# Kernel tuning notes

Measured on AMD Instinct MI355X. Metric: run time of the kernel, lower is better.

## Reference

```python
import jax, jax.numpy as jnp
import numpy as np

CROSSOVER_MAGNITUDE = 0.3
MUTATION_FACTOR = 0.3

B, A, H = 16, 512, 8  # batch, activation_size (== dim_emb), n_head


def setup_inputs() -> dict:
    key = jax.random.key(0)
    ks = jax.random.split(key, 11)
    d = A
    s = 0.02  # small init scale for weights
    return {
        "Q": jax.random.normal(ks[0], (B, A, A), jnp.float32),
        "K": jax.random.normal(ks[1], (B, A, A), jnp.float32),
        "V": jax.random.normal(ks[2], (B, A), jnp.float32),
        "WQ_w": jax.random.normal(ks[3], (d, d), jnp.float32) * s,
        "WQ_b": jax.random.normal(ks[4], (d,), jnp.float32) * s,
        "WK_w": jax.random.normal(ks[5], (d, d), jnp.float32) * s,
        "WK_b": jax.random.normal(ks[6], (d,), jnp.float32) * s,
        "WV_w": jax.random.normal(ks[7], (d, d), jnp.float32) * s,
        "WV_b": jax.random.normal(ks[8], (d,), jnp.float32) * s,
        "WO_w": jax.random.normal(ks[9], (d, d * H), jnp.float32) * s,
        "WO_b": jax.random.normal(ks[10], (d,), jnp.float32) * s,
    }


def _attention_core(Qp, Kp, Vp, WO_w, WO_b):
    # Qp, Kp: (B, A, A) projected; identical across heads in the original
    # (heads are copies stacked before shared Linear), so compute once
    # and broadcast. Vp: (B, A).
    rkey = jax.random.key(42)
    kp, km, kr1, kr2 = jax.random.split(rkey, 4)

    am0 = jnp.einsum('bji,bjk->bik', Qp, Kp) / jnp.sqrt(jnp.float32(8.0))
    am = jnp.broadcast_to(am0[:, None], (B, H, A, A))  # (B,H,A,A)

    def mutate(a):
        # elementwise multiply by U(1-mf, 1+mf) noise
        m = jax.random.uniform(km, a.shape, jnp.float32,
                               1.0 - MUTATION_FACTOR, 1.0 + MUTATION_FACTOR)
        return a * m

    def crossover(a):
        # swap the tail segments [c:] of two random rows per (batch, head)
        c = A - int(A * CROSSOVER_MAGNITUDE)
        r1 = jax.random.randint(kr1, (B, H), 0, A)
        r2 = jax.random.randint(kr2, (B, H), 0, A)
        bi = jnp.arange(B)[:, None]
        hi = jnp.arange(H)[None, :]
        tails = a[..., c:]                     # (B,H,A,A-c)
        t1 = tails[bi, hi, r1]                 # (B,H,A-c)
        t2 = tails[bi, hi, r2]
        tails = tails.at[bi, hi, r1].set(t2).at[bi, hi, r2].set(t1)
        return jnp.concatenate([a[..., :c], tails], axis=-1)

    p = jax.random.uniform(kp, ())
    am = jax.lax.cond(p <= 0.6, mutate, crossover, am)

    attn = jax.nn.softmax(am, axis=-1)               # (B,H,A,A)
    out = jnp.einsum('bhij,bj->bhi', attn, Vp)       # attn @ V[...,None] squeezed
    out = out.reshape(B, H * A)
    return out @ WO_w.T + WO_b                       # (B, A)


def reference(Q, K, V, WQ_w, WQ_b, WK_w, WK_b, WV_w, WV_b, WO_w, WO_b):
    Qp = Q @ WQ_w.T + WQ_b   # (B,A,A), same for every head
    Kp = K @ WK_w.T + WK_b
    Vp = V @ WV_w.T + WV_b   # (B,A)
    return _attention_core(Qp, Kp, Vp, WO_w, WO_b)
```

## Files before the change

### kernel.cpp

```cpp
#include <hip/hip_runtime.h>
#include <stdint.h>
#include <string.h>

#define B_ 16
#define A_ 512
#define H_ 8
#define C_CROSS 359
#define LDSTRIDE 40

typedef short short8 __attribute__((ext_vector_type(8)));
typedef unsigned short us8 __attribute__((ext_vector_type(8)));
typedef float floatx4 __attribute__((ext_vector_type(4)));

__host__ __device__ __forceinline__ uint32_t rotl32(uint32_t x, int r) {
#ifdef __HIP_DEVICE_COMPILE__
  return __builtin_amdgcn_alignbit(x, x, 32 - r);
#else
  return (x << r) | (x >> (32 - r));
#endif
}

__host__ __device__ __forceinline__ void tf2x32(uint32_t k0, uint32_t k1,
                                                uint32_t x0, uint32_t x1,
                                                uint32_t& o0, uint32_t& o1) {
  uint32_t ks2 = k0 ^ k1 ^ 0x1BD11BDAu;
  x0 += k0; x1 += k1;
#define TFR(r) { x0 += x1; x1 = rotl32(x1, r); x1 ^= x0; }
  TFR(13) TFR(15) TFR(26) TFR(6)   x0 += k1;  x1 += ks2 + 1u;
  TFR(17) TFR(29) TFR(16) TFR(24)  x0 += ks2; x1 += k0 + 2u;
  TFR(13) TFR(15) TFR(26) TFR(6)   x0 += k0;  x1 += k1 + 3u;
  TFR(17) TFR(29) TFR(16) TFR(24)  x0 += k1;  x1 += ks2 + 4u;
  TFR(13) TFR(15) TFR(26) TFR(6)   x0 += ks2; x1 += k0 + 5u;
#undef TFR
  o0 = x0; o1 = x1;
}

__host__ __device__ __forceinline__ float bits2u01(uint32_t bits) {
  uint32_t v = (bits >> 9) | 0x3f800000u;
  float f;
#ifdef __HIP_DEVICE_COMPILE__
  f = __uint_as_float(v);
#else
  memcpy(&f, &v, 4);
#endif
  return f - 1.0f;
}

__device__ __forceinline__ float exp2_native(float x) {
  float r;
  asm("v_exp_f32 %0, %1\n\ts_nop 0" : "=v"(r) : "v"(x));
  return r;
}

__device__ __forceinline__ void tsplit(float x, short& h, short& l) {
  uint32_t u = __float_as_uint(x);
  float hf = __uint_as_float(u & 0xffff0000u);
  h = (short)(u >> 16);
  l = (short)(__float_as_uint(x - hf) >> 16);
}

__device__ __forceinline__ void tsplit8(const float4& v0, const float4& v1,
                                        short8& h, short8& l) {
  float xs[8] = {v0.x, v0.y, v0.z, v0.w, v1.x, v1.y, v1.z, v1.w};
#pragma unroll
  for (int j = 0; j < 8; ++j) {
    short hh, ll;
    tsplit(xs[j], hh, ll);
    h[j] = hh; l[j] = ll;
  }
}

__device__ __forceinline__ void genmul_chunk(ushort* __restrict__ mbits, int chunk,
                                             uint32_t km0, uint32_t km1) {
  int t = threadIdx.x;
  uint32_t base = (uint32_t)chunk * 16384u;
#pragma unroll
  for (int j = 0; j < 8; ++j) {
    uint32_t L0 = base + (uint32_t)j * 2048u + (uint32_t)t * 8u;
    us8 out;
#pragma unroll
    for (int q = 0; q < 8; ++q) {
      uint32_t o0, o1;
      tf2x32(km0, km1, 0u, L0 + (uint32_t)q, o0, o1);
      out[q] = (unsigned short)((o0 ^ o1) >> 16);
    }
    *(us8*)(mbits + L0) = out;
  }
}

__global__ __launch_bounds__(256) void presplitW(
    const float* __restrict__ Wq, ushort* __restrict__ WqH, ushort* __restrict__ WqL,
    const float* __restrict__ Wk, ushort* __restrict__ WkH, ushort* __restrict__ WkL) {
  int gid = blockIdx.x * 256 + threadIdx.x;
  int z = gid >> 15;
  size_t e0 = (size_t)(gid & 32767) * 8;
  const float* W = z ? Wk : Wq;
  ushort* WH = z ? WkH : WqH;
  ushort* WL = z ? WkL : WqL;
  float4 v0 = *(const float4*)(W + e0);
  float4 v1 = *(const float4*)(W + e0 + 4);
  short8 h8, l8;
  tsplit8(v0, v1, h8, l8);
  *(short8*)(WH + e0) = h8;
  *(short8*)(WL + e0) = l8;
}

__global__ __launch_bounds__(256, 2) void lin3(
    const float* __restrict__ Xq,
    const ushort* __restrict__ WqH, const ushort* __restrict__ WqL,
    const float* __restrict__ bq, ushort* __restrict__ QptH, ushort* __restrict__ QptL,
    const float* __restrict__ Xk,
    const ushort* __restrict__ WkH, const ushort* __restrict__ WkL,
    const float* __restrict__ bk, ushort* __restrict__ KptH, ushort* __restrict__ KptL,
    ushort* __restrict__ mbits, int genOff, uint32_t km0, uint32_t km1) {
  int bid = blockIdx.x;
  if (bid >= 512) {
    genmul_chunk(mbits, genOff + (bid - 512), km0, km1);
    return;
  }
  int z = bid >> 8;
  int rem = bid & 255;
  int ti = rem >> 2, tn = rem & 3;
  const float* X = z ? Xk : Xq;
  const ushort* WH = z ? WkH : WqH;
  const ushort* WL = z ? WkL : WqL;
  const float* bias = z ? bk : bq;
  ushort* OH = z ? KptH : QptH;
  ushort* OL = z ? KptL : QptL;

  __shared__ __align__(16) char smem[40960];
  ushort (*Ah)[LDSTRIDE] = (ushort(*)[LDSTRIDE])(smem);
  ushort (*Al)[LDSTRIDE] = (ushort(*)[LDSTRIDE])(smem + 10240);
  ushort (*Bh)[LDSTRIDE] = (ushort(*)[LDSTRIDE])(smem + 20480);
  ushort (*Bl)[LDSTRIDE] = (ushort(*)[LDSTRIDE])(smem + 30720);
  uint32_t (*cs)[132] = (uint32_t(*)[132])(smem);

  int tid = threadIdx.x;
  int w = tid >> 6, lane = tid & 63, quad = lane >> 4, l16 = lane & 15;
  int wm = (w >> 1) * 64, wn = (w & 1) * 64;
  int m0 = ti * 128;
  int n0 = tn * 128;

  float bv[4];
#pragma unroll
  for (int nt = 0; nt < 4; ++nt) bv[nt] = bias[n0 + wn + nt * 16 + l16];

  const float* pX[2];
  const ushort* pWH[2];
  const ushort* pWL[2];
  int mW[2], kgW[2];
#pragma unroll
  for (int g = 0; g < 2; ++g) {
    int gid = g * 256 + tid;
    int m = gid >> 2, kg = gid & 3;
    mW[g] = m; kgW[g] = kg;
    pX[g] = X + (size_t)(m0 + m) * 512 + kg * 8;
    size_t woff = (size_t)(n0 + m) * 512 + kg * 8;
    pWH[g] = WH + woff;
    pWL[g] = WL + woff;
  }

  float4 ra[2][2];
  short8 rbh[2], rbl[2];
#pragma unroll
  for (int g = 0; g < 2; ++g) {
    ra[g][0] = *(const float4*)(pX[g]);
    ra[g][1] = *(const float4*)(pX[g] + 4);
    rbh[g] = *(const short8*)(pWH[g]);
    rbl[g] = *(const short8*)(pWL[g]);
  }

  floatx4 acc[4][4] = {};

  for (int k0 = 0; k0 < 512; k0 += 32) {
    __syncthreads();
#pragma unroll
    for (int g = 0; g < 2; ++g) {
      short8 h8, l8;
      tsplit8(ra[g][0], ra[g][1], h8, l8);
      *(short8*)&Ah[mW[g]][kgW[g] * 8] = h8;
      *(short8*)&Al[mW[g]][kgW[g] * 8] = l8;
      *(short8*)&Bh[mW[g]][kgW[g] * 8] = rbh[g];
      *(short8*)&Bl[mW[g]][kgW[g] * 8] = rbl[g];
    }
    __syncthreads();
    if (k0 < 480) {
      int kn = k0 + 32;
#pragma unroll
      for (int g = 0; g < 2; ++g) {
        ra[g][0] = *(const float4*)(pX[g] + kn);
        ra[g][1] = *(const float4*)(pX[g] + kn + 4);
        rbh[g] = *(const short8*)(pWH[g] + kn);
        rbl[g] = *(const short8*)(pWL[g] + kn);
      }
    }
    short8 fAh[4], fAl[4], fBh[4], fBl[4];
#pragma unroll
    for (int t4 = 0; t4 < 4; ++t4) {
      int ma = wm + t4 * 16 + l16;
      int nb = wn + t4 * 16 + l16;
      fAh[t4] = *(const short8*)&Ah[ma][quad * 8];
      fAl[t4] = *(const short8*)&Al[ma][quad * 8];
      fBh[t4] = *(const short8*)&Bh[nb][quad * 8];
      fBl[t4] = *(const short8*)&Bl[nb][quad * 8];
    }
#pragma unroll
    for (int mt = 0; mt < 4; ++mt)
#pragma unroll
      for (int nt = 0; nt < 4; ++nt) {
        acc[mt][nt] = __builtin_amdgcn_mfma_f32_16x16x32_bf16(fAh[mt], fBh[nt], acc[mt][nt], 0, 0, 0);
        acc[mt][nt] = __builtin_amdgcn_mfma_f32_16x16x32_bf16(fAh[mt], fBl[nt], acc[mt][nt], 0, 0, 0);
        acc[mt][nt] = __builtin_amdgcn_mfma_f32_16x16x32_bf16(fAl[mt], fBh[nt], acc[mt][nt], 0, 0, 0);
      }
  }

  __syncthreads();
  int bb = m0 >> 9, i0 = m0 & 511;
  for (int p = 0; p < 2; ++p) {
    if ((w & 1) == p) {
#pragma unroll
      for (int mt = 0; mt < 4; ++mt)
#pragma unroll
        for (int nt = 0; nt < 4; ++nt)
#pragma unroll
          for (int rr = 0; rr < 4; ++rr) {
            float val = acc[mt][nt][rr] + bv[nt];
            uint32_t u = __float_as_uint(val);
            uint32_t hi = u & 0xffff0000u;
            uint32_t lo = __float_as_uint(val - __uint_as_float(hi)) >> 16;
            cs[nt * 16 + l16][wm + mt * 16 + quad * 4 + rr] = hi | lo;
          }
    }
    __syncthreads();
    {
      int col_l = tid >> 2, iseg = (tid & 3) * 32;
      int d = n0 + p * 64 + col_l;
      size_t obase = ((size_t)(bb * 512 + d)) * 512 + i0 + iseg;
      ushort* oh = OH + obase;
      ushort* ol = OL + obase;
#pragma unroll
      for (int sgi = 0; sgi < 4; ++sgi) {
        short8 hv, lv;
#pragma unroll
        for (int j = 0; j < 8; ++j) {
          uint32_t v = cs[col_l][iseg + sgi * 8 + j];
          hv[j] = (short)(v >> 16);
          lv[j] = (short)(v & 0xffffu);
        }
        *(short8*)(oh + sgi * 8) = hv;
        *(short8*)(ol + sgi * 8) = lv;
      }
    }
    __syncthreads();
  }
}

__global__ __launch_bounds__(256, 2) void lin_mfma2(
    const float* __restrict__ Xq, const float* __restrict__ Wq,
    const float* __restrict__ bq, ushort* __restrict__ QptH, ushort* __restrict__ QptL,
    const float* __restrict__ Xk, const float* __restrict__ Wk,
    const float* __restrict__ bk, ushort* __restrict__ KptH, ushort* __restrict__ KptL) {
  int bid = blockIdx.x;
  int z = bid >> 8;
  int rem = bid & 255;
  int ti = rem >> 2, tn = rem & 3;
  const float* X = z ? Xk : Xq;
  const float* W = z ? Wk : Wq;
  const float* bias = z ? bk : bq;
  ushort* OH = z ? KptH : QptH;
  ushort* OL = z ? KptL : QptL;

  __shared__ __align__(16) char smem[40960];
  ushort (*Ah)[LDSTRIDE] = (ushort(*)[LDSTRIDE])(smem);
  ushort (*Al)[LDSTRIDE] = (ushort(*)[LDSTRIDE])(smem + 10240);
  ushort (*Bh)[LDSTRIDE] = (ushort(*)[LDSTRIDE])(smem + 20480);
  ushort (*Bl)[LDSTRIDE] = (ushort(*)[LDSTRIDE])(smem + 30720);
  uint32_t (*cs)[132] = (uint32_t(*)[132])(smem);

  int tid = threadIdx.x;
  int w = tid >> 6, lane = tid & 63, quad = lane >> 4, l16 = lane & 15;
  int wm = (w >> 1) * 64, wn = (w & 1) * 64;
  int m0 = ti * 128;
  int n0 = tn * 128;

  float bv[4];
#pragma unroll
  for (int nt = 0; nt < 4; ++nt) bv[nt] = bias[n0 + wn + nt * 16 + l16];

  const float* pX[2];
  const float* pW[2];
  int mW[2], kgW[2];
#pragma unroll
  for (int g = 0; g < 2; ++g) {
    int gid = g * 256 + tid;
    int m = gid >> 2, kg = gid & 3;
    mW[g] = m; kgW[g] = kg;
    pX[g] = X + (size_t)(m0 + m) * 512 + kg * 8;
    pW[g] = W + (size_t)(n0 + m) * 512 + kg * 8;
  }

  float4 ra[2][2], rb[2][2];
#pragma unroll
  for (int g = 0; g < 2; ++g) {
    ra[g][0] = *(const float4*)(pX[g]);
    ra[g][1] = *(const float4*)(pX[g] + 4);
    rb[g][0] = *(const float4*)(pW[g]);
    rb[g][1] = *(const float4*)(pW[g] + 4);
  }

  floatx4 acc[4][4] = {};

  for (int k0 = 0; k0 < 512; k0 += 32) {
    __syncthreads();
#pragma unroll
    for (int g = 0; g < 2; ++g) {
      short8 h8, l8;
      tsplit8(ra[g][0], ra[g][1], h8, l8);
      *(short8*)&Ah[mW[g]][kgW[g] * 8] = h8;
      *(short8*)&Al[mW[g]][kgW[g] * 8] = l8;
      tsplit8(rb[g][0], rb[g][1], h8, l8);
      *(short8*)&Bh[mW[g]][kgW[g] * 8] = h8;
      *(short8*)&Bl[mW[g]][kgW[g] * 8] = l8;
    }
    __syncthreads();
    if (k0 < 480) {
      int kn = k0 + 32;
#pragma unroll
      for (int g = 0; g < 2; ++g) {
        ra[g][0] = *(const float4*)(pX[g] + kn);
        ra[g][1] = *(const float4*)(pX[g] + kn + 4);
        rb[g][0] = *(const float4*)(pW[g] + kn);
        rb[g][1] = *(const float4*)(pW[g] + kn + 4);
      }
    }
    short8 fAh[4], fAl[4], fBh[4], fBl[4];
#pragma unroll
    for (int t4 = 0; t4 < 4; ++t4) {
      int ma = wm + t4 * 16 + l16;
      int nb = wn + t4 * 16 + l16;
      fAh[t4] = *(const short8*)&Ah[ma][quad * 8];
      fAl[t4] = *(const short8*)&Al[ma][quad * 8];
      fBh[t4] = *(const short8*)&Bh[nb][quad * 8];
      fBl[t4] = *(const short8*)&Bl[nb][quad * 8];
    }
#pragma unroll
    for (int mt = 0; mt < 4; ++mt)
#pragma unroll
      for (int nt = 0; nt < 4; ++nt) {
        acc[mt][nt] = __builtin_amdgcn_mfma_f32_16x16x32_bf16(fAh[mt], fBh[nt], acc[mt][nt], 0, 0, 0);
        acc[mt][nt] = __builtin_amdgcn_mfma_f32_16x16x32_bf16(fAh[mt], fBl[nt], acc[mt][nt], 0, 0, 0);
        acc[mt][nt] = __builtin_amdgcn_mfma_f32_16x16x32_bf16(fAl[mt], fBh[nt], acc[mt][nt], 0, 0, 0);
      }
  }

  __syncthreads();
  int bb = m0 >> 9, i0 = m0 & 511;
  for (int p = 0; p < 2; ++p) {
    if ((w & 1) == p) {
#pragma unroll
      for (int mt = 0; mt < 4; ++mt)
#pragma unroll
        for (int nt = 0; nt < 4; ++nt)
#pragma unroll
          for (int rr = 0; rr < 4; ++rr) {
            float val = acc[mt][nt][rr] + bv[nt];
            uint32_t u = __float_as_uint(val);
            uint32_t hi = u & 0xffff0000u;
            uint32_t lo = __float_as_uint(val - __uint_as_float(hi)) >> 16;
            cs[nt * 16 + l16][wm + mt * 16 + quad * 4 + rr] = hi | lo;
          }
    }
    __syncthreads();
    {
      int col_l = tid >> 2, iseg = (tid & 3) * 32;
      int d = n0 + p * 64 + col_l;
      size_t obase = ((size_t)(bb * 512 + d)) * 512 + i0 + iseg;
      ushort* oh = OH + obase;
      ushort* ol = OL + obase;
#pragma unroll
      for (int sgi = 0; sgi < 4; ++sgi) {
        short8 hv, lv;
#pragma unroll
        for (int j = 0; j < 8; ++j) {
          uint32_t v = cs[col_l][iseg + sgi * 8 + j];
          hv[j] = (short)(v >> 16);
          lv[j] = (short)(v & 0xffffu);
        }
        *(short8*)(oh + sgi * 8) = hv;
        *(short8*)(ol + sgi * 8) = lv;
      }
    }
    __syncthreads();
  }
}

__global__ __launch_bounds__(256, 2) void am3(
    const ushort* __restrict__ QH, const ushort* __restrict__ QL,
    const ushort* __restrict__ KH, const ushort* __restrict__ KL,
    float* __restrict__ am0,
    ushort* __restrict__ mbits, int genOff, uint32_t km0, uint32_t km1) {
  int bid = blockIdx.x;
  if (bid >= 256) {
    genmul_chunk(mbits, genOff + (bid - 256), km0, km1);
    return;
  }
  int xcd = bid & 7, slot = bid >> 3;
  int bz = xcd + 8 * (slot >> 4);
  int tt = slot & 15, ti = tt >> 2, tk = tt & 3;
  int bm0 = ti * 128, bn0 = tk * 128;
  size_t base = (size_t)bz * 262144;

  __shared__ __align__(16) char smem[40960];
  ushort (*Ah)[LDSTRIDE] = (ushort(*)[LDSTRIDE])(smem);
  ushort (*Al)[LDSTRIDE] = (ushort(*)[LDSTRIDE])(smem + 10240);
  ushort (*Bh)[LDSTRIDE] = (ushort(*)[LDSTRIDE])(smem + 20480);
  ushort (*Bl)[LDSTRIDE] = (ushort(*)[LDSTRIDE])(smem + 30720);

  int tid = threadIdx.x;
  int w = tid >> 6, lane = tid & 63, quad = lane >> 4, l16 = lane & 15;
  int wm = (w >> 1) * 64, wn = (w & 1) * 64;

  const ushort *pAH[2], *pAL[2], *pBH[2], *pBL[2];
  int mW[2], kgW[2];
#pragma unroll
  for (int g = 0; g < 2; ++g) {
    int gid = g * 256 + tid;
    int m = gid >> 2, kg = gid & 3;
    mW[g] = m; kgW[g] = kg;
    size_t offA = base + (size_t)(bm0 + m) * 512 + kg * 8;
    size_t offB = base + (size_t)(bn0 + m) * 512 + kg * 8;
    pAH[g] = QH + offA; pAL[g] = QL + offA;
    pBH[g] = KH + offB; pBL[g] = KL + offB;
  }

  short8 rah[2], ral[2], rbh[2], rbl[2];
#pragma unroll
  for (int g = 0; g < 2; ++g) {
    rah[g] = *(const short8*)(pAH[g]);
    ral[g] = *(const short8*)(pAL[g]);
    rbh[g] = *(const short8*)(pBH[g]);
    rbl[g] = *(const short8*)(pBL[g]);
  }

  floatx4 acc[4][4] = {};

  for (int k0 = 0; k0 < 512; k0 += 32) {
    __syncthreads();
#pragma unroll
    for (int g = 0; g < 2; ++g) {
      *(short8*)&Ah[mW[g]][kgW[g] * 8] = rah[g];
      *(short8*)&Al[mW[g]][kgW[g] * 8] = ral[g];
      *(short8*)&Bh[mW[g]][kgW[g] * 8] = rbh[g];
      *(short8*)&Bl[mW[g]][kgW[g] * 8] = rbl[g];
    }
    __syncthreads();
    if (k0 < 480) {
      int kn = k0 + 32;
#pragma unroll
      for (int g = 0; g < 2; ++g) {
        rah[g] = *(const short8*)(pAH[g] + kn);
        ral[g] = *(const short8*)(pAL[g] + kn);
        rbh[g] = *(const short8*)(pBH[g] + kn);
        rbl[g] = *(const short8*)(pBL[g] + kn);
      }
    }
    short8 fAh[4], fAl[4], fBh[4], fBl[4];
#pragma unroll
    for (int t4 = 0; t4 < 4; ++t4) {
      int ma = wm + t4 * 16 + l16;
      int nb = wn + t4 * 16 + l16;
      fAh[t4] = *(const short8*)&Ah[ma][quad * 8];
      fAl[t4] = *(const short8*)&Al[ma][quad * 8];
      fBh[t4] = *(const short8*)&Bh[nb][quad * 8];
      fBl[t4] = *(const short8*)&Bl[nb][quad * 8];
    }
#pragma unroll
    for (int mt = 0; mt < 4; ++mt)
#pragma unroll
      for (int nt = 0; nt < 4; ++nt) {
        acc[mt][nt] = __builtin_amdgcn_mfma_f32_16x16x32_bf16(fAh[mt], fBh[nt], acc[mt][nt], 0, 0, 0);
        acc[mt][nt] = __builtin_amdgcn_mfma_f32_16x16x32_bf16(fAh[mt], fBl[nt], acc[mt][nt], 0, 0, 0);
        acc[mt][nt] = __builtin_amdgcn_mfma_f32_16x16x32_bf16(fAl[mt], fBh[nt], acc[mt][nt], 0, 0, 0);
      }
  }
  const float scale = 0.35355339059327373f;
#pragma unroll
  for (int mt = 0; mt < 4; ++mt)
#pragma unroll
    for (int nt = 0; nt < 4; ++nt)
#pragma unroll
      for (int rr = 0; rr < 4; ++rr) {
        int row = bm0 + wm + mt * 16 + quad * 4 + rr;
        int col = bn0 + wn + nt * 16 + l16;
        am0[((size_t)(bz * 512 + row)) * 512 + col] = acc[mt][nt][rr] * scale;
      }
}

__global__ __launch_bounds__(256) void small_gemm(
    const float* __restrict__ X, const float* __restrict__ W,
    const float* __restrict__ bias, float* __restrict__ out, int K) {
  __shared__ float xs[16 * 260];
  __shared__ float ws[16 * 260];
  int tid = threadIdx.x;
  int j0 = blockIdx.x * 16;
  int k0 = blockIdx.y * 256;
#pragma unroll
  for (int it = 0; it < 4; ++it) {
    int idx = it * 256 + tid;
    int rr = idx >> 6, kk4 = idx & 63;
    float4 xv = *(const float4*)(X + (size_t)rr * K + k0 + kk4 * 4);
    float4 wv = *(const float4*)(W + (size_t)(j0 + rr) * K + k0 + kk4 * 4);
    *(float4*)&xs[rr * 260 + kk4 * 4] = xv;
    *(float4*)&ws[rr * 260 + kk4 * 4] = wv;
  }
  __syncthreads();
  int b = tid & 15, j = tid >> 4;
  const float* xr = &xs[b * 260];
  const float* wr = &ws[j * 260];
  float acc = 0.f;
#pragma unroll
  for (int kk = 0; kk < 256; kk += 4) {
    float4 a = *(const float4*)(xr + kk);
    float4 w4 = *(const float4*)(wr + kk);
    acc += a.x * w4.x + a.y * w4.y + a.z * w4.z + a.w * w4.w;
  }
  if (blockIdx.y == 0) acc += bias[j0 + j];
  atomicAdd(&out[b * 512 + j0 + j], acc);
}

__global__ __launch_bounds__(256) void soft_mut_pre(
    const float* __restrict__ am0, const float* __restrict__ Vp,
    const ushort* __restrict__ mbits, float* __restrict__ oa) {
  int tid = threadIdx.x;
  int w = tid >> 6, lane = tid & 63;
  int rrow = blockIdx.x * 4 + w;
  int b = rrow >> 9, i = rrow & 511;
  int k0 = lane * 8;
  const float* ar = am0 + (((size_t)rrow) << 9) + k0;
  const float* vr = Vp + (b << 9) + k0;
  float4 a0 = *(const float4*)ar, a1 = *(const float4*)(ar + 4);
  float4 v0 = *(const float4*)vr, v1 = *(const float4*)(vr + 4);
  const float LOG2E = 1.4426950408889634f;
  float a2[8] = {a0.x * LOG2E, a0.y * LOG2E, a0.z * LOG2E, a0.w * LOG2E,
                 a1.x * LOG2E, a1.y * LOG2E, a1.z * LOG2E, a1.w * LOG2E};
  float vv[8] = {v0.x, v0.y, v0.z, v0.w, v1.x, v1.y, v1.z, v1.w};
  float outv[8];
#pragma unroll
  for (int h = 0; h < 8; ++h) {
    us8 mb = *(const us8*)(mbits + ((((size_t)(b * 8 + h)) << 18) + ((size_t)i << 9) + k0));
    float s = 0.f, wsum = 0.f;
#pragma unroll
    for (int j = 0; j < 8; ++j) {
      uint32_t fb = (((uint32_t)mb[j]) << 7) | 0x3f800000u;
      float f = __uint_as_float(fb);
      float m = fmaxf(0.7f, __builtin_fmaf(f, 0.6f, 0.1f));
      float e = exp2_native(a2[j] * m);
      s += e;
      wsum += e * vv[j];
    }
#pragma unroll
    for (int o = 32; o; o >>= 1) { s += __shfl_xor(s, o); wsum += __shfl_xor(wsum, o); }
    outv[h] = wsum / s;
  }
  if (lane == 0) {
    int ob = (b << 12) + i;
#pragma unroll
    for (int h = 0; h < 8; ++h) oa[ob + (h << 9)] = outv[h];
  }
}

__global__ __launch_bounds__(256) void soft_mut(
    const float* __restrict__ am0, const float* __restrict__ Vp,
    float* __restrict__ oa, uint32_t km0, uint32_t km1) {
  int tid = threadIdx.x;
  int w = tid >> 6, lane = tid & 63;
  int rrow = blockIdx.x * 4 + w;
  int b = rrow >> 9, i = rrow & 511;
  int k0 = lane * 8;
  const float* ar = am0 + (((size_t)rrow) << 9) + k0;
  const float* vr = Vp + (b << 9) + k0;
  float4 a0 = *(const float4*)ar, a1 = *(const float4*)(ar + 4);
  float4 v0 = *(const float4*)vr, v1 = *(const float4*)(vr + 4);
  const float LOG2E = 1.4426950408889634f;
  float a2[8] = {a0.x * LOG2E, a0.y * LOG2E, a0.z * LOG2E, a0.w * LOG2E,
                 a1.x * LOG2E, a1.y * LOG2E, a1.z * LOG2E, a1.w * LOG2E};
  float vv[8] = {v0.x, v0.y, v0.z, v0.w, v1.x, v1.y, v1.z, v1.w};
  uint32_t Lbase = (uint32_t)b * 2097152u + (uint32_t)i * 512u + (uint32_t)k0;
  float outv[8];
#pragma unroll
  for (int h = 0; h < 8; ++h) {
    uint32_t Lh = Lbase + (uint32_t)h * 262144u;
    float s = 0.f, wsum = 0.f;
#pragma unroll
    for (int j = 0; j < 8; ++j) {
      uint32_t o0, o1;
      tf2x32(km0, km1, 0u, Lh + (uint32_t)j, o0, o1);
      uint32_t bits = o0 ^ o1;
      float f = __uint_as_float((bits >> 9) | 0x3f800000u);
      float m = fmaxf(0.7f, __builtin_fmaf(f, 0.6f, 0.1f));
      float e = exp2_native(a2[j] * m);
      s += e;
      wsum += e * vv[j];
    }
#pragma unroll
    for (int o = 32; o; o >>= 1) { s += __shfl_xor(s, o); wsum += __shfl_xor(wsum, o); }
    outv[h] = wsum / s;
  }
  if (lane == 0) {
    int ob = (b << 12) + i;
#pragma unroll
    for (int h = 0; h < 8; ++h) oa[ob + (h << 9)] = outv[h];
  }
}

struct CrossCfg { int r1[B_ * H_]; int r2[B_ * H_]; };

__global__ __launch_bounds__(256) void soft_cross(
    const float* __restrict__ am0, const float* __restrict__ Vp,
    float* __restrict__ oa, CrossCfg cfg) {
  int tid = threadIdx.x;
  int w = tid >> 6, lane = tid & 63;
  int rrow = blockIdx.x * 4 + w;
  int b = rrow >> 12, h = (rrow >> 9) & 7, i = rrow & 511;
  int rr1 = cfg.r1[b * 8 + h], rr2 = cfg.r2[b * 8 + h];
  int src = (i == rr2) ? rr1 : ((i == rr1) ? rr2 : i);
  const float* ar = am0 + ((size_t)((b << 9) + i)) * A_;
  const float* ar2 = am0 + ((size_t)((b << 9) + src)) * A_;
  const float* vr = Vp + (b << 9);
  float s = 0.f, wsum = 0.f;
#pragma unroll
  for (int j = 0; j < 8; ++j) {
    int k = lane + 64 * j;
    float x = (k >= C_CROSS) ? ar2[k] : ar[k];
    float e = __expf(x);
    s += e;
    wsum += e * vr[k];
  }
#pragma unroll
  for (int o = 32; o; o >>= 1) { s += __shfl_xor(s, o); wsum += __shfl_xor(wsum, o); }
  if (lane == 0) oa[(((size_t)(b * 8 + h)) << 9) + i] = wsum / s;
}

extern "C" void kernel_launch(void* const* d_in, const int* in_sizes, int n_in,
                              void* d_out, int out_size, void* d_ws, size_t ws_size,
                              hipStream_t stream) {
  (void)in_sizes; (void)n_in; (void)out_size;
  const float* Q    = (const float*)d_in[0];
  const float* K    = (const float*)d_in[1];
  const float* V    = (const float*)d_in[2];
  const float* WQ_w = (const float*)d_in[3];
  const float* WQ_b = (const float*)d_in[4];
  const float* WK_w = (const float*)d_in[5];
  const float* WK_b = (const float*)d_in[6];
  const float* WV_w = (const float*)d_in[7];
  const float* WV_b = (const float*)d_in[8];
  const float* WO_w = (const float*)d_in[9];
  const float* WO_b = (const float*)d_in[10];
  float* out = (float*)d_out;

  char* ws = (char*)d_ws;
  ushort* QptH = (ushort*)(ws);
  ushort* QptL = (ushort*)(ws + (size_t)8388608);
  ushort* KptH = (ushort*)(ws + (size_t)16777216);
  ushort* KptL = (ushort*)(ws + (size_t)25165824);
  float*  am0  = (float*) (ws + (size_t)33554432);
  float*  Vp   = (float*) (ws + (size_t)50331648);
  float*  oa   = (float*) (ws + (size_t)50397184);
  ushort* WqH  = (ushort*)(ws + (size_t)50659328);
  ushort* WqL  = (ushort*)(ws + (size_t)51183616);
  ushort* WkH  = (ushort*)(ws + (size_t)51707904);
  ushort* WkL  = (ushort*)(ws + (size_t)52232192);
  ushort* mbits= (ushort*)(ws + (size_t)52756480);

  int tier = (ws_size >= (size_t)119865344) ? 0
           : (ws_size >= (size_t)52756480) ? 1 : 2;

  uint32_t kp0, kp1, km0, km1, kr10, kr11, kr20, kr21, a, bbits;
  tf2x32(0u, 42u, 0u, 0u, kp0, kp1);
  tf2x32(0u, 42u, 0u, 1u, km0, km1);
  tf2x32(0u, 42u, 0u, 2u, kr10, kr11);
  tf2x32(0u, 42u, 0u, 3u, kr20, kr21);
  tf2x32(kp0, kp1, 0u, 0u, a, bbits);
  float p = bits2u01(a ^ bbits);
  if (p < 0.f) p = 0.f;
  bool mutate = (p <= 0.6f);

  hipMemsetAsync(Vp, 0, 16 * 512 * sizeof(float), stream);
  hipMemsetAsync(out, 0, 16 * 512 * sizeof(float), stream);

  if (tier <= 1) {
    presplitW<<<256, 256, 0, stream>>>(WQ_w, WqH, WqL, WK_w, WkH, WkL);
    int linGrid = (tier == 0 && mutate) ? 512 + 1024 : 512;
    lin3<<<linGrid, 256, 0, stream>>>(Q, WqH, WqL, WQ_b, QptH, QptL,
                                      K, WkH, WkL, WK_b, KptH, KptL,
                                      mbits, 0, km0, km1);
  } else {
    lin_mfma2<<<512, 256, 0, stream>>>(Q, WQ_w, WQ_b, QptH, QptL,
                                       K, WK_w, WK_b, KptH, KptL);
  }
  small_gemm<<<dim3(32, 2), 256, 0, stream>>>(V, WV_w, WV_b, Vp, 512);
  {
    int amGrid = (tier == 0 && mutate) ? 256 + 1024 : 256;
    am3<<<amGrid, 256, 0, stream>>>(QptH, QptL, KptH, KptL, am0,
                                    mbits, 1024, km0, km1);
  }
  if (mutate) {
    if (tier == 0)
      soft_mut_pre<<<2048, 256, 0, stream>>>(am0, Vp, mbits, oa);
    else
      soft_mut<<<2048, 256, 0, stream>>>(am0, Vp, oa, km0, km1);
  } else {
    CrossCfg cfg;
    uint32_t c0, c1;
    tf2x32(kr10, kr11, 0u, 1u, c0, c1);
    for (int t = 0; t < B_ * H_; ++t) {
      tf2x32(c0, c1, 0u, (uint32_t)t, a, bbits);
      cfg.r1[t] = (int)((a ^ bbits) & 511u);
    }
    tf2x32(kr20, kr21, 0u, 1u, c0, c1);
    for (int t = 0; t < B_ * H_; ++t) {
      tf2x32(c0, c1, 0u, (uint32_t)t, a, bbits);
      cfg.r2[t] = (int)((a ^ bbits) & 511u);
    }
    soft_cross<<<16384, 256, 0, stream>>>(am0, Vp, oa, cfg);
  }
  small_gemm<<<dim3(32, 16), 256, 0, stream>>>(oa, WO_w, WO_b, out, 4096);
}
```

Before: 222.2 us.

## Fuse whole pipeline into one persistent kernel with grid-wide barriers

Replaces the sequence of presplit, projection, score GEMM, mutated softmax and output GEMM launches with a single persistent kernel of 512 blocks. Stages are separated by atomic-counter grid barriers in workspace. The RNG mask generation and the V projection are folded into the first stage. This removes per-launch overhead and the gaps between kernels, but it relies on all 512 blocks being co-resident and replaces launch boundaries with spin barriers. Workspace-tier fallback paths are also reworked so that the bf16 split weights are always pre-split.

```diff
diff --git a/kernel.cpp b/kernel.cpp
--- a/kernel.cpp
+++ b/kernel.cpp
@@ -7,6 +7,7 @@
 #define H_ 8
 #define C_CROSS 359
 #define LDSTRIDE 40
+#define NBLK 512
 
 typedef short short8 __attribute__((ext_vector_type(8)));
 typedef unsigned short us8 __attribute__((ext_vector_type(8)));
@@ -52,25 +53,19 @@
   return r;
 }
 
-__device__ __forceinline__ void tsplit(float x, short& h, short& l) {
-  uint32_t u = __float_as_uint(x);
-  float hf = __uint_as_float(u & 0xffff0000u);
-  h = (short)(u >> 16);
-  l = (short)(__float_as_uint(x - hf) >> 16);
-}
-
 __device__ __forceinline__ void tsplit8(const float4& v0, const float4& v1,
                                         short8& h, short8& l) {
   float xs[8] = {v0.x, v0.y, v0.z, v0.w, v1.x, v1.y, v1.z, v1.w};
 #pragma unroll
   for (int j = 0; j < 8; ++j) {
-    short hh, ll;
-    tsplit(xs[j], hh, ll);
-    h[j] = hh; l[j] = ll;
-  }
-}
-
-__device__ __forceinline__ void genmul_chunk(ushort* __restrict__ mbits, int chunk,
+    uint32_t u = __float_as_uint(xs[j]);
+    float hf = __uint_as_float(u & 0xffff0000u);
+    h[j] = (short)(u >> 16);
+    l[j] = (short)(__float_as_uint(xs[j] - hf) >> 16);
+  }
+}
+
+__device__ __forceinline__ void genmul_chunk(ushort* mbits, int chunk,
                                              uint32_t km0, uint32_t km1) {
   int t = threadIdx.x;
   uint32_t base = (uint32_t)chunk * 16384u;
@@ -85,6 +80,380 @@
       out[q] = (unsigned short)((o0 ^ o1) >> 16);
     }
     *(us8*)(mbits + L0) = out;
+  }
+}
+
+__global__ __launch_bounds__(256, 2) void mega(
+    const float* Q, const float* WQ_w, const float* WQ_b,
+    const float* K, const float* WK_w, const float* WK_b,
+    const float* V, const float* WV_w, const float* WV_b,
+    const float* WO_w, const float* WO_b, float* out,
+    ushort* QptH, ushort* QptL, ushort* KptH, ushort* KptL,
+    ushort* WqH, ushort* WqL, ushort* WkH, ushort* WkL,
+    float* am0, float* Vp, float* oa, ushort* mbits, int* bar,
+    uint32_t km0, uint32_t km1) {
+  __shared__ __align__(16) char smem[40960];
+  int tid = threadIdx.x;
+  int w = tid >> 6, lane = tid & 63, quad = lane >> 4, l16 = lane & 15;
+
+  auto gbar = [&](int idx) {
+    __syncthreads();
+    __threadfence();
+    if (tid == 0) {
+      atomicAdd(&bar[idx], 1);
+      while (atomicAdd(&bar[idx], 0) < NBLK) { __builtin_amdgcn_s_sleep(2); }
+    }
+    __syncthreads();
+    __threadfence();
+  };
+
+  for (int job = blockIdx.x; job < 2368; job += NBLK) {
+    if (job < 256) {
+      int gid = job * 256 + tid;
+      int z = gid >> 15;
+      size_t e0 = (size_t)(gid & 32767) * 8;
+      const float* W = z ? WK_w : WQ_w;
+      ushort* WH = z ? WkH : WqH;
+      ushort* WL = z ? WkL : WqL;
+      float4 v0 = *(const float4*)(W + e0);
+      float4 v1 = *(const float4*)(W + e0 + 4);
+      short8 h8, l8;
+      tsplit8(v0, v1, h8, l8);
+      *(short8*)(WH + e0) = h8;
+      *(short8*)(WL + e0) = l8;
+    } else if (job < 320) {
+      int v = job - 256;
+      int j0 = (v >> 1) * 16, k0 = (v & 1) * 256;
+      float* xs = (float*)smem;
+      float* wsh = (float*)(smem + 16640);
+      __syncthreads();
+#pragma unroll
+      for (int it = 0; it < 4; ++it) {
+        int idx = it * 256 + tid;
+        int rr = idx >> 6, kk4 = idx & 63;
+        float4 xv = *(const float4*)(V + (size_t)rr * 512 + k0 + kk4 * 4);
+        float4 wv = *(const float4*)(WV_w + (size_t)(j0 + rr) * 512 + k0 + kk4 * 4);
+        *(float4*)&xs[rr * 260 + kk4 * 4] = xv;
+        *(float4*)&wsh[rr * 260 + kk4 * 4] = wv;
+      }
+      __syncthreads();
+      int b = tid & 15, j = tid >> 4;
+      const float* xr = &xs[b * 260];
+      const float* wr = &wsh[j * 260];
+      float acc = 0.f;
+#pragma unroll
+      for (int kk = 0; kk < 256; kk += 4) {
+        float4 a = *(const float4*)(xr + kk);
+        float4 w4 = *(const float4*)(wr + kk);
+        acc += a.x * w4.x + a.y * w4.y + a.z * w4.z + a.w * w4.w;
+      }
+      if ((v & 1) == 0) acc += WV_b[j0 + j];
+      atomicAdd(&Vp[b * 512 + j0 + j], acc);
+      __syncthreads();
+    } else {
+      genmul_chunk(mbits, job - 320, km0, km1);
+    }
+  }
+  gbar(0);
+
+  {
+    int job = blockIdx.x;
+    int z = job >> 8;
+    int rem = job & 255;
+    int ti = rem >> 2, tn = rem & 3;
+    const float* X = z ? K : Q;
+    const ushort* WH = z ? WkH : WqH;
+    const ushort* WL = z ? WkL : WqL;
+    const float* bias = z ? WK_b : WQ_b;
+    ushort* OH = z ? KptH : QptH;
+    ushort* OL = z ? KptL : QptL;
+
+    ushort (*Ah)[LDSTRIDE] = (ushort(*)[LDSTRIDE])(smem);
+    ushort (*Al)[LDSTRIDE] = (ushort(*)[LDSTRIDE])(smem + 10240);
+    ushort (*Bh)[LDSTRIDE] = (ushort(*)[LDSTRIDE])(smem + 20480);
+    ushort (*Bl)[LDSTRIDE] = (ushort(*)[LDSTRIDE])(smem + 30720);
+    uint32_t (*cs)[132] = (uint32_t(*)[132])(smem);
+
+    int wm = (w >> 1) * 64, wn = (w & 1) * 64;
+    int m0 = ti * 128, n0 = tn * 128;
+
+    float bv[4];
+#pragma unroll
+    for (int nt = 0; nt < 4; ++nt) bv[nt] = bias[n0 + wn + nt * 16 + l16];
+
+    const float* pX[2];
+    const ushort* pWH[2];
+    const ushort* pWL[2];
+    int mW[2], kgW[2];
+#pragma unroll
+    for (int g = 0; g < 2; ++g) {
+      int gid = g * 256 + tid;
+      int m = gid >> 2, kg = gid & 3;
+      mW[g] = m; kgW[g] = kg;
+      pX[g] = X + (size_t)(m0 + m) * 512 + kg * 8;
+      size_t woff = (size_t)(n0 + m) * 512 + kg * 8;
+      pWH[g] = WH + woff;
+      pWL[g] = WL + woff;
+    }
+
+    float4 ra[2][2];
+    short8 rbh[2], rbl[2];
+#pragma unroll
+    for (int g = 0; g < 2; ++g) {
+      ra[g][0] = *(const float4*)(pX[g]);
+      ra[g][1] = *(const float4*)(pX[g] + 4);
+      rbh[g] = *(const short8*)(pWH[g]);
+      rbl[g] = *(const short8*)(pWL[g]);
+    }
+
+    floatx4 acc[4][4] = {};
+
+    for (int k0 = 0; k0 < 512; k0 += 32) {
+      __syncthreads();
+#pragma unroll
+      for (int g = 0; g < 2; ++g) {
+        short8 h8, l8;
+        tsplit8(ra[g][0], ra[g][1], h8, l8);
+        *(short8*)&Ah[mW[g]][kgW[g] * 8] = h8;
+        *(short8*)&Al[mW[g]][kgW[g] * 8] = l8;
+        *(short8*)&Bh[mW[g]][kgW[g] * 8] = rbh[g];
+        *(short8*)&Bl[mW[g]][kgW[g] * 8] = rbl[g];
+      }
+      __syncthreads();
+      if (k0 < 480) {
+        int kn = k0 + 32;
+#pragma unroll
+        for (int g = 0; g < 2; ++g) {
+          ra[g][0] = *(const float4*)(pX[g] + kn);
+          ra[g][1] = *(const float4*)(pX[g] + kn + 4);
+          rbh[g] = *(const short8*)(pWH[g] + kn);
+          rbl[g] = *(const short8*)(pWL[g] + kn);
+        }
+      }
+      short8 fAh[4], fAl[4], fBh[4], fBl[4];
+#pragma unroll
+      for (int t4 = 0; t4 < 4; ++t4) {
+        int ma = wm + t4 * 16 + l16;
+        int nb = wn + t4 * 16 + l16;
+        fAh[t4] = *(const short8*)&Ah[ma][quad * 8];
+        fAl[t4] = *(const short8*)&Al[ma][quad * 8];
+        fBh[t4] = *(const short8*)&Bh[nb][quad * 8];
+        fBl[t4] = *(const short8*)&Bl[nb][quad * 8];
+      }
+#pragma unroll
+      for (int mt = 0; mt < 4; ++mt)
+#pragma unroll
+        for (int nt = 0; nt < 4; ++nt) {
+          acc[mt][nt] = __builtin_amdgcn_mfma_f32_16x16x32_bf16(fAh[mt], fBh[nt], acc[mt][nt], 0, 0, 0);
+          acc[mt][nt] = __builtin_amdgcn_mfma_f32_16x16x32_bf16(fAh[mt], fBl[nt], acc[mt][nt], 0, 0, 0);
+          acc[mt][nt] = __builtin_amdgcn_mfma_f32_16x16x32_bf16(fAl[mt], fBh[nt], acc[mt][nt], 0, 0, 0);
+        }
+    }
+
+    __syncthreads();
+    int bb = m0 >> 9, i0 = m0 & 511;
+    for (int p = 0; p < 2; ++p) {
+      if ((w & 1) == p) {
+#pragma unroll
+        for (int mt = 0; mt < 4; ++mt)
+#pragma unroll
+          for (int nt = 0; nt < 4; ++nt)
+#pragma unroll
+            for (int rr = 0; rr < 4; ++rr) {
+              float val = acc[mt][nt][rr] + bv[nt];
+              uint32_t u = __float_as_uint(val);
+              uint32_t hi = u & 0xffff0000u;
+              uint32_t lo = __float_as_uint(val - __uint_as_float(hi)) >> 16;
+              cs[nt * 16 + l16][wm + mt * 16 + quad * 4 + rr] = hi | lo;
+            }
+      }
+      __syncthreads();
+      {
+        int col_l = tid >> 2, iseg = (tid & 3) * 32;
+        int d = n0 + p * 64 + col_l;
+        size_t obase = ((size_t)(bb * 512 + d)) * 512 + i0 + iseg;
+        ushort* oh = OH + obase;
+        ushort* ol = OL + obase;
+#pragma unroll
+        for (int sgi = 0; sgi < 4; ++sgi) {
+          short8 hv, lv;
+#pragma unroll
+          for (int j = 0; j < 8; ++j) {
+            uint32_t v = cs[col_l][iseg + sgi * 8 + j];
+            hv[j] = (short)(v >> 16);
+            lv[j] = (short)(v & 0xffffu);
+          }
+          *(short8*)(oh + sgi * 8) = hv;
+          *(short8*)(ol + sgi * 8) = lv;
+        }
+      }
+      __syncthreads();
+    }
+  }
+  gbar(1);
+
+  {
+    int job = blockIdx.x;
+    int half = job & 1, tile = job >> 1;
+    int xcd = tile & 7, slot = tile >> 3;
+    int bz = xcd + 8 * (slot >> 4);
+    int tt = slot & 15, ti = tt >> 2, tk = tt & 3;
+    int bm0 = ti * 128 + half * 64, bn0 = tk * 128;
+    size_t base = (size_t)bz * 262144;
+
+    ushort (*Ah)[LDSTRIDE] = (ushort(*)[LDSTRIDE])(smem);
+    ushort (*Al)[LDSTRIDE] = (ushort(*)[LDSTRIDE])(smem + 5120);
+    ushort (*Bh)[LDSTRIDE] = (ushort(*)[LDSTRIDE])(smem + 10240);
+    ushort (*Bl)[LDSTRIDE] = (ushort(*)[LDSTRIDE])(smem + 20480);
+
+    int wm = (w >> 1) * 32, wn = (w & 1) * 64;
+
+    int smA = tid >> 2, skgA = tid & 3;
+    const ushort* pAH = QptH + base + (size_t)(bm0 + smA) * 512 + skgA * 8;
+    const ushort* pAL = QptL + base + (size_t)(bm0 + smA) * 512 + skgA * 8;
+    const ushort* pBH[2];
+    const ushort* pBL[2];
+    int mB[2], kgB[2];
+#pragma unroll
+    for (int g = 0; g < 2; ++g) {
+      int gid = g * 256 + tid;
+      mB[g] = gid >> 2; kgB[g] = gid & 3;
+      size_t offB = base + (size_t)(bn0 + mB[g]) * 512 + kgB[g] * 8;
+      pBH[g] = KptH + offB; pBL[g] = KptL + offB;
+    }
+
+    short8 rah = *(const short8*)pAH, ral = *(const short8*)pAL;
+    short8 rbh[2], rbl[2];
+#pragma unroll
+    for (int g = 0; g < 2; ++g) {
+      rbh[g] = *(const short8*)(pBH[g]);
+      rbl[g] = *(const short8*)(pBL[g]);
+    }
+
+    floatx4 acc[2][4] = {};
+
+    for (int k0 = 0; k0 < 512; k0 += 32) {
+      __syncthreads();
+      *(short8*)&Ah[smA][skgA * 8] = rah;
+      *(short8*)&Al[smA][skgA * 8] = ral;
+#pragma unroll
+      for (int g = 0; g < 2; ++g) {
+        *(short8*)&Bh[mB[g]][kgB[g] * 8] = rbh[g];
+        *(short8*)&Bl[mB[g]][kgB[g] * 8] = rbl[g];
+      }
+      __syncthreads();
+      if (k0 < 480) {
+        int kn = k0 + 32;
+        rah = *(const short8*)(pAH + kn);
+        ral = *(const short8*)(pAL + kn);
+#pragma unroll
+        for (int g = 0; g < 2; ++g) {
+          rbh[g] = *(const short8*)(pBH[g] + kn);
+          rbl[g] = *(const short8*)(pBL[g] + kn);
+        }
+      }
+      short8 fAh[2], fAl[2], fBh[4], fBl[4];
+#pragma unroll
+      for (int mt = 0; mt < 2; ++mt) {
+        int ma = wm + mt * 16 + l16;
+        fAh[mt] = *(const short8*)&Ah[ma][quad * 8];
+        fAl[mt] = *(const short8*)&Al[ma][quad * 8];
+      }
+#pragma unroll
+      for (int nt = 0; nt < 4; ++nt) {
+        int nb = wn + nt * 16 + l16;
+        fBh[nt] = *(const short8*)&Bh[nb][quad * 8];
+        fBl[nt] = *(const short8*)&Bl[nb][quad * 8];
+      }
+#pragma unroll
+      for (int mt = 0; mt < 2; ++mt)
+#pragma unroll
+        for (int nt = 0; nt < 4; ++nt) {
+          acc[mt][nt] = __builtin_amdgcn_mfma_f32_16x16x32_bf16(fAh[mt], fBh[nt], acc[mt][nt], 0, 0, 0);
+          acc[mt][nt] = __builtin_amdgcn_mfma_f32_16x16x32_bf16(fAh[mt], fBl[nt], acc[mt][nt], 0, 0, 0);
+          acc[mt][nt] = __builtin_amdgcn_mfma_f32_16x16x32_bf16(fAl[mt], fBh[nt], acc[mt][nt], 0, 0, 0);
+        }
+    }
+    const float scale = 0.35355339059327373f;
+#pragma unroll
+    for (int mt = 0; mt < 2; ++mt)
+#pragma unroll
+      for (int nt = 0; nt < 4; ++nt)
+#pragma unroll
+        for (int rr = 0; rr < 4; ++rr) {
+          int row = bm0 + wm + mt * 16 + quad * 4 + rr;
+          int col = bn0 + wn + nt * 16 + l16;
+          am0[((size_t)(bz * 512 + row)) * 512 + col] = acc[mt][nt][rr] * scale;
+        }
+  }
+  gbar(2);
+
+  for (int g4 = blockIdx.x; g4 < 2048; g4 += NBLK) {
+    int rrow = g4 * 4 + w;
+    int b = rrow >> 9, i = rrow & 511;
+    int k0 = lane * 8;
+    const float* ar = am0 + (((size_t)rrow) << 9) + k0;
+    const float* vr = Vp + (b << 9) + k0;
+    float4 a0 = *(const float4*)ar, a1 = *(const float4*)(ar + 4);
+    float4 v0 = *(const float4*)vr, v1 = *(const float4*)(vr + 4);
+    const float LOG2E = 1.4426950408889634f;
+    float a2[8] = {a0.x * LOG2E, a0.y * LOG2E, a0.z * LOG2E, a0.w * LOG2E,
+                   a1.x * LOG2E, a1.y * LOG2E, a1.z * LOG2E, a1.w * LOG2E};
+    float vv[8] = {v0.x, v0.y, v0.z, v0.w, v1.x, v1.y, v1.z, v1.w};
+    float outv[8];
+#pragma unroll
+    for (int h = 0; h < 8; ++h) {
+      us8 mb = *(const us8*)(mbits + ((((size_t)(b * 8 + h)) << 18) + ((size_t)i << 9) + k0));
+      float s = 0.f, wsum = 0.f;
+#pragma unroll
+      for (int j = 0; j < 8; ++j) {
+        uint32_t fb = (((uint32_t)mb[j]) << 7) | 0x3f800000u;
+        float f = __uint_as_float(fb);
+        float m = fmaxf(0.7f, __builtin_fmaf(f, 0.6f, 0.1f));
+        float e = exp2_native(a2[j] * m);
+        s += e;
+        wsum += e * vv[j];
+      }
+#pragma unroll
+      for (int o = 32; o; o >>= 1) { s += __shfl_xor(s, o); wsum += __shfl_xor(wsum, o); }
+      outv[h] = wsum / s;
+    }
+    if (lane == 0) {
+      int ob = (b << 12) + i;
+#pragma unroll
+      for (int h = 0; h < 8; ++h) oa[ob + (h << 9)] = outv[h];
+    }
+  }
+  gbar(3);
+
+  {
+    int job = blockIdx.x;
+    int j0 = (job & 31) * 16, kc = job >> 5, k0 = kc * 256;
+    float* xs = (float*)smem;
+    float* wsh = (float*)(smem + 16640);
+    __syncthreads();
+#pragma unroll
+    for (int it = 0; it < 4; ++it) {
+      int idx = it * 256 + tid;
+      int rr = idx >> 6, kk4 = idx & 63;
+      float4 xv = *(const float4*)(oa + (size_t)rr * 4096 + k0 + kk4 * 4);
+      float4 wv = *(const float4*)(WO_w + (size_t)(j0 + rr) * 4096 + k0 + kk4 * 4);
+      *(float4*)&xs[rr * 260 + kk4 * 4] = xv;
+      *(float4*)&wsh[rr * 260 + kk4 * 4] = wv;
+    }
+    __syncthreads();
+    int b = tid & 15, j = tid >> 4;
+    const float* xr = &xs[b * 260];
+    const float* wr = &wsh[j * 260];
+    float acc = 0.f;
+#pragma unroll
+    for (int kk = 0; kk < 256; kk += 4) {
+      float4 a = *(const float4*)(xr + kk);
+      float4 w4 = *(const float4*)(wr + kk);
+      acc += a.x * w4.x + a.y * w4.y + a.z * w4.z + a.w * w4.w;
+    }
+    if (kc == 0) acc += WO_b[j0 + j];
+    atomicAdd(&out[b * 512 + j0 + j], acc);
   }
 }
 
@@ -111,13 +480,8 @@
     const float* __restrict__ bq, ushort* __restrict__ QptH, ushort* __restrict__ QptL,
     const float* __restrict__ Xk,
     const ushort* __restrict__ WkH, const ushort* __restrict__ WkL,
-    const float* __restrict__ bk, ushort* __restrict__ KptH, ushort* __restrict__ KptL,
-    ushort* __restrict__ mbits, int genOff, uint32_t km0, uint32_t km1) {
+    const float* __restrict__ bk, ushort* __restrict__ KptH, ushort* __restrict__ KptL) {
   int bid = blockIdx.x;
-  if (bid >= 512) {
-    genmul_chunk(mbits, genOff + (bid - 512), km0, km1);
-    return;
-  }
   int z = bid >> 8;
   int rem = bid & 255;
   int ti = rem >> 2, tn = rem & 3;
@@ -138,8 +502,7 @@
   int tid = threadIdx.x;
   int w = tid >> 6, lane = tid & 63, quad = lane >> 4, l16 = lane & 15;
   int wm = (w >> 1) * 64, wn = (w & 1) * 64;
-  int m0 = ti * 128;
-  int n0 = tn * 128;
+  int m0 = ti * 128, n0 = tn * 128;
 
   float bv[4];
 #pragma unroll
@@ -255,155 +618,11 @@
   }
 }
 
-__global__ __launch_bounds__(256, 2) void lin_mfma2(
-    const float* __restrict__ Xq, const float* __restrict__ Wq,
-    const float* __restrict__ bq, ushort* __restrict__ QptH, ushort* __restrict__ QptL,
-    const float* __restrict__ Xk, const float* __restrict__ Wk,
-    const float* __restrict__ bk, ushort* __restrict__ KptH, ushort* __restrict__ KptL) {
-  int bid = blockIdx.x;
-  int z = bid >> 8;
-  int rem = bid & 255;
-  int ti = rem >> 2, tn = rem & 3;
-  const float* X = z ? Xk : Xq;
-  const float* W = z ? Wk : Wq;
-  const float* bias = z ? bk : bq;
-  ushort* OH = z ? KptH : QptH;
-  ushort* OL = z ? KptL : QptL;
-
-  __shared__ __align__(16) char smem[40960];
-  ushort (*Ah)[LDSTRIDE] = (ushort(*)[LDSTRIDE])(smem);
-  ushort (*Al)[LDSTRIDE] = (ushort(*)[LDSTRIDE])(smem + 10240);
-  ushort (*Bh)[LDSTRIDE] = (ushort(*)[LDSTRIDE])(smem + 20480);
-  ushort (*Bl)[LDSTRIDE] = (ushort(*)[LDSTRIDE])(smem + 30720);
-  uint32_t (*cs)[132] = (uint32_t(*)[132])(smem);
-
-  int tid = threadIdx.x;
-  int w = tid >> 6, lane = tid & 63, quad = lane >> 4, l16 = lane & 15;
-  int wm = (w >> 1) * 64, wn = (w & 1) * 64;
-  int m0 = ti * 128;
-  int n0 = tn * 128;
-
-  float bv[4];
-#pragma unroll
-  for (int nt = 0; nt < 4; ++nt) bv[nt] = bias[n0 + wn + nt * 16 + l16];
-
-  const float* pX[2];
-  const float* pW[2];
-  int mW[2], kgW[2];
-#pragma unroll
-  for (int g = 0; g < 2; ++g) {
-    int gid = g * 256 + tid;
-    int m = gid >> 2, kg = gid & 3;
-    mW[g] = m; kgW[g] = kg;
-    pX[g] = X + (size_t)(m0 + m) * 512 + kg * 8;
-    pW[g] = W + (size_t)(n0 + m) * 512 + kg * 8;
-  }
-
-  float4 ra[2][2], rb[2][2];
-#pragma unroll
-  for (int g = 0; g < 2; ++g) {
-    ra[g][0] = *(const float4*)(pX[g]);
-    ra[g][1] = *(const float4*)(pX[g] + 4);
-    rb[g][0] = *(const float4*)(pW[g]);
-    rb[g][1] = *(const float4*)(pW[g] + 4);
-  }
-
-  floatx4 acc[4][4] = {};
-
-  for (int k0 = 0; k0 < 512; k0 += 32) {
-    __syncthreads();
-#pragma unroll
-    for (int g = 0; g < 2; ++g) {
-      short8 h8, l8;
-      tsplit8(ra[g][0], ra[g][1], h8, l8);
-      *(short8*)&Ah[mW[g]][kgW[g] * 8] = h8;
-      *(short8*)&Al[mW[g]][kgW[g] * 8] = l8;
-      tsplit8(rb[g][0], rb[g][1], h8, l8);
-      *(short8*)&Bh[mW[g]][kgW[g] * 8] = h8;
-      *(short8*)&Bl[mW[g]][kgW[g] * 8] = l8;
-    }
-    __syncthreads();
-    if (k0 < 480) {
-      int kn = k0 + 32;
-#pragma unroll
-      for (int g = 0; g < 2; ++g) {
-        ra[g][0] = *(const float4*)(pX[g] + kn);
-        ra[g][1] = *(const float4*)(pX[g] + kn + 4);
-        rb[g][0] = *(const float4*)(pW[g] + kn);
-        rb[g][1] = *(const float4*)(pW[g] + kn + 4);
-      }
-    }
-    short8 fAh[4], fAl[4], fBh[4], fBl[4];
-#pragma unroll
-    for (int t4 = 0; t4 < 4; ++t4) {
-      int ma = wm + t4 * 16 + l16;
-      int nb = wn + t4 * 16 + l16;
-      fAh[t4] = *(const short8*)&Ah[ma][quad * 8];
-      fAl[t4] = *(const short8*)&Al[ma][quad * 8];
-      fBh[t4] = *(const short8*)&Bh[nb][quad * 8];
-      fBl[t4] = *(const short8*)&Bl[nb][quad * 8];
-    }
-#pragma unroll
-    for (int mt = 0; mt < 4; ++mt)
-#pragma unroll
-      for (int nt = 0; nt < 4; ++nt) {
-        acc[mt][nt] = __builtin_amdgcn_mfma_f32_16x16x32_bf16(fAh[mt], fBh[nt], acc[mt][nt], 0, 0, 0);
-        acc[mt][nt] = __builtin_amdgcn_mfma_f32_16x16x32_bf16(fAh[mt], fBl[nt], acc[mt][nt], 0, 0, 0);
-        acc[mt][nt] = __builtin_amdgcn_mfma_f32_16x16x32_bf16(fAl[mt], fBh[nt], acc[mt][nt], 0, 0, 0);
-      }
-  }
-
-  __syncthreads();
-  int bb = m0 >> 9, i0 = m0 & 511;
-  for (int p = 0; p < 2; ++p) {
-    if ((w & 1) == p) {
-#pragma unroll
-      for (int mt = 0; mt < 4; ++mt)
-#pragma unroll
-        for (int nt = 0; nt < 4; ++nt)
-#pragma unroll
-          for (int rr = 0; rr < 4; ++rr) {
-            float val = acc[mt][nt][rr] + bv[nt];
-            uint32_t u = __float_as_uint(val);
-            uint32_t hi = u & 0xffff0000u;
-            uint32_t lo = __float_as_uint(val - __uint_as_float(hi)) >> 16;
-            cs[nt * 16 + l16][wm + mt * 16 + quad * 4 + rr] = hi | lo;
-          }
-    }
-    __syncthreads();
-    {
-      int col_l = tid >> 2, iseg = (tid & 3) * 32;
-      int d = n0 + p * 64 + col_l;
-      size_t obase = ((size_t)(bb * 512 + d)) * 512 + i0 + iseg;
-      ushort* oh = OH + obase;
-      ushort* ol = OL + obase;
-#pragma unroll
-      for (int sgi = 0; sgi < 4; ++sgi) {
-        short8 hv, lv;
-#pragma unroll
-        for (int j = 0; j < 8; ++j) {
-          uint32_t v = cs[col_l][iseg + sgi * 8 + j];
-          hv[j] = (short)(v >> 16);
-          lv[j] = (short)(v & 0xffffu);
-        }
-        *(short8*)(oh + sgi * 8) = hv;
-        *(short8*)(ol + sgi * 8) = lv;
-      }
-    }
-    __syncthreads();
-  }
-}
-
 __global__ __launch_bounds__(256, 2) void am3(
     const ushort* __restrict__ QH, const ushort* __restrict__ QL,
     const ushort* __restrict__ KH, const ushort* __restrict__ KL,
-    float* __restrict__ am0,
-    ushort* __restrict__ mbits, int genOff, uint32_t km0, uint32_t km1) {
+    float* __restrict__ am0) {
   int bid = blockIdx.x;
-  if (bid >= 256) {
-    genmul_chunk(mbits, genOff + (bid - 256), km0, km1);
-    return;
-  }
   int xcd = bid & 7, slot = bid >> 3;
   int bz = xcd + 8 * (slot >> 4);
   int tt = slot & 15, ti = tt >> 2, tk = tt & 3;
@@ -526,47 +745,6 @@
   }
   if (blockIdx.y == 0) acc += bias[j0 + j];
   atomicAdd(&out[b * 512 + j0 + j], acc);
-}
-
-__global__ __launch_bounds__(256) void soft_mut_pre(
-    const float* __restrict__ am0, const float* __restrict__ Vp,
-    const ushort* __restrict__ mbits, float* __restrict__ oa) {
-  int tid = threadIdx.x;
-  int w = tid >> 6, lane = tid & 63;
-  int rrow = blockIdx.x * 4 + w;
-  int b = rrow >> 9, i = rrow & 511;
-  int k0 = lane * 8;
-  const float* ar = am0 + (((size_t)rrow) << 9) + k0;
-  const float* vr = Vp + (b << 9) + k0;
-  float4 a0 = *(const float4*)ar, a1 = *(const float4*)(ar + 4);
-  float4 v0 = *(const float4*)vr, v1 = *(const float4*)(vr + 4);
-  const float LOG2E = 1.4426950408889634f;
-  float a2[8] = {a0.x * LOG2E, a0.y * LOG2E, a0.z * LOG2E, a0.w * LOG2E,
-                 a1.x * LOG2E, a1.y * LOG2E, a1.z * LOG2E, a1.w * LOG2E};
-  float vv[8] = {v0.x, v0.y, v0.z, v0.w, v1.x, v1.y, v1.z, v1.w};
-  float outv[8];
-#pragma unroll
-  for (int h = 0; h < 8; ++h) {
-    us8 mb = *(const us8*)(mbits + ((((size_t)(b * 8 + h)) << 18) + ((size_t)i << 9) + k0));
-    float s = 0.f, wsum = 0.f;
-#pragma unroll
-    for (int j = 0; j < 8; ++j) {
-      uint32_t fb = (((uint32_t)mb[j]) << 7) | 0x3f800000u;
-      float f = __uint_as_float(fb);
-      float m = fmaxf(0.7f, __builtin_fmaf(f, 0.6f, 0.1f));
-      float e = exp2_native(a2[j] * m);
-      s += e;
-      wsum += e * vv[j];
-    }
-#pragma unroll
-    for (int o = 32; o; o >>= 1) { s += __shfl_xor(s, o); wsum += __shfl_xor(wsum, o); }
-    outv[h] = wsum / s;
-  }
-  if (lane == 0) {
-    int ob = (b << 12) + i;
-#pragma unroll
-    for (int h = 0; h < 8; ++h) oa[ob + (h << 9)] = outv[h];
-  }
 }
 
 __global__ __launch_bounds__(256) void soft_mut(
@@ -665,6 +843,7 @@
   ushort* KptL = (ushort*)(ws + (size_t)25165824);
   float*  am0  = (float*) (ws + (size_t)33554432);
   float*  Vp   = (float*) (ws + (size_t)50331648);
+  int*    bar  = (int*)   (ws + (size_t)50364416);
   float*  oa   = (float*) (ws + (size_t)50397184);
   ushort* WqH  = (ushort*)(ws + (size_t)50659328);
   ushort* WqL  = (ushort*)(ws + (size_t)51183616);
@@ -685,30 +864,34 @@
   if (p < 0.f) p = 0.f;
   bool mutate = (p <= 0.6f);
 
-  hipMemsetAsync(Vp, 0, 16 * 512 * sizeof(float), stream);
+  hipMemsetAsync(ws + (size_t)50331648, 0, 33024, stream);
   hipMemsetAsync(out, 0, 16 * 512 * sizeof(float), stream);
+
+  if (mutate && tier == 0) {
+    mega<<<NBLK, 256, 0, stream>>>(
+        Q, WQ_w, WQ_b, K, WK_w, WK_b, V, WV_w, WV_b, WO_w, WO_b, out,
+        QptH, QptL, KptH, KptL, WqH, WqL, WkH, WkL,
+        am0, Vp, oa, mbits, bar, km0, km1);
+    return;
+  }
 
   if (tier <= 1) {
     presplitW<<<256, 256, 0, stream>>>(WQ_w, WqH, WqL, WK_w, WkH, WkL);
-    int linGrid = (tier == 0 && mutate) ? 512 + 1024 : 512;
-    lin3<<<linGrid, 256, 0, stream>>>(Q, WqH, WqL, WQ_b, QptH, QptL,
-                                      K, WkH, WkL, WK_b, KptH, KptL,
-                                      mbits, 0, km0, km1);
+    lin3<<<512, 256, 0, stream>>>(Q, WqH, WqL, WQ_b, QptH, QptL,
+                                  K, WkH, WkL, WK_b, KptH, KptL);
   } else {
-    lin_mfma2<<<512, 256, 0, stream>>>(Q, WQ_w, WQ_b, QptH, QptL,
-                                       K, WK_w, WK_b, KptH, KptL);
+    ushort* tWqH = (ushort*)(ws + (size_t)33554432);
+    ushort* tWqL = tWqH + 262144;
+    ushort* tWkH = tWqL + 262144;
+    ushort* tWkL = tWkH + 262144;
+    presplitW<<<256, 256, 0, stream>>>(WQ_w, tWqH, tWqL, WK_w, tWkH, tWkL);
+    lin3<<<512, 256, 0, stream>>>(Q, tWqH, tWqL, WQ_b, QptH, QptL,
+                                  K, tWkH, tWkL, WK_b, KptH, KptL);
   }
   small_gemm<<<dim3(32, 2), 256, 0, stream>>>(V, WV_w, WV_b, Vp, 512);
-  {
-    int amGrid = (tier == 0 && mutate) ? 256 + 1024 : 256;
-    am3<<<amGrid, 256, 0, stream>>>(QptH, QptL, KptH, KptL, am0,
-                                    mbits, 1024, km0, km1);
-  }
+  am3<<<256, 256, 0, stream>>>(QptH, QptL, KptH, KptL, am0);
   if (mutate) {
-    if (tier == 0)
-      soft_mut_pre<<<2048, 256, 0, stream>>>(am0, Vp, mbits, oa);
-    else
-      soft_mut<<<2048, 256, 0, stream>>>(am0, Vp, oa, km0, km1);
+    soft_mut<<<2048, 256, 0, stream>>>(am0, Vp, oa, km0, km1);
   } else {
     CrossCfg cfg;
     uint32_t c0, c1;
```

Result: slower. 699.1 us (+214.7%).
